# Optimization experiments

Hardware: AMD Instinct MI355X
Metric: run time of the kernel (lower is better)

Reference implementation:

```python
import jax, jax.numpy as jnp
import numpy as np

NUM_EXPERTS = 32
HIDDEN = 2048
INTER = 768
TOP_K = 4
B, S = 2, 512


def setup_inputs() -> dict:
    key = jax.random.key(0)
    k1, k2, k3, k4, k5 = jax.random.split(key, 5)
    hidden_states = jax.random.normal(k1, (B, S, HIDDEN), dtype=jnp.float32)
    routing_weights = jax.random.uniform(k2, (B, S, NUM_EXPERTS), dtype=jnp.float32)
    gate_up_proj = jax.random.normal(k3, (NUM_EXPERTS, HIDDEN, 2 * INTER), dtype=jnp.float32) * 0.02
    down_proj = jax.random.normal(k4, (NUM_EXPERTS, INTER, HIDDEN), dtype=jnp.float32) * 0.02
    router_indices = jax.random.randint(k5, (B, S, TOP_K), 0, NUM_EXPERTS, dtype=jnp.int64)
    return {
        "hidden_states": hidden_states,
        "routing_weights": routing_weights,
        "gate_up_proj": gate_up_proj,
        "down_proj": down_proj,
        "router_indices": router_indices,
    }


def reference(hidden_states, routing_weights, gate_up_proj, down_proj, router_indices):
    b, s, h = hidden_states.shape
    e = gate_up_proj.shape[0]
    x = hidden_states.reshape(-1, h)                       # [T, H]
    ri = router_indices.reshape(-1, router_indices.shape[-1])  # [T, K]
    rw = routing_weights.reshape(-1, e)                    # [T, E]
    # token-expert membership: expert applied once per token iff it appears in top-k
    member = (ri[:, :, None] == jnp.arange(e)[None, None, :]).any(axis=1)  # [T, E] bool
    combine_w = jnp.where(member, rw, 0.0)                 # [T, E]
    # dense grouped-GEMM reference: compute every expert for every token, mask-combine
    gate_up = jnp.einsum("th,ehg->teg", x, gate_up_proj)   # [T, E, 2I]
    gate, up = jnp.split(gate_up, 2, axis=-1)              # [T, E, I] each
    act = jax.nn.silu(gate) * up                           # SwiGLU
    act = act * combine_w[:, :, None]                      # fold combine weights pre-down-proj
    out = jnp.einsum("tei,eih->th", act, down_proj)        # [T, H]
    return out.reshape(b, s, h)
```

## Files before the change

### kernel.cpp

```cpp
#include <hip/hip_runtime.h>
#include <hip/hip_bf16.h>

#define NUM_EXPERTS 32
#define HIDDEN 2048
#define INTER 768
#define TOPK 4
#define T_TOKENS 1024
#define CAP 1024

#define MW 192
#define BK 64
#define LSTR 72

typedef __bf16 bf16x8 __attribute__((ext_vector_type(8)));
typedef float floatx4 __attribute__((ext_vector_type(4)));

__device__ __forceinline__ int swz(int row, int kq) {
    return row * LSTR + (((kq ^ (row >> 2)) & 7) << 3);
}

__global__ void route_kernel(const int* __restrict__ ri, int* __restrict__ counts,
                             int* __restrict__ tok_list) {
    int t = blockIdx.x * blockDim.x + threadIdx.x;
    if (t >= T_TOKENS) return;
    int idx[TOPK];
#pragma unroll
    for (int j = 0; j < TOPK; ++j) idx[j] = ri[t * TOPK + j];
#pragma unroll
    for (int j = 0; j < TOPK; ++j) {
        int e = idx[j];
        bool dup = false;
#pragma unroll
        for (int l = 0; l < TOPK; ++l)
            if (l < j && idx[l] == e) dup = true;
        if (!dup) {
            int s = atomicAdd(&counts[e], 1);
            tok_list[e * CAP + s] = t;
        }
    }
}

__global__ __launch_bounds__(256) void conv_kernel(const float* __restrict__ x,
                                                   __bf16* __restrict__ xb) {
    int i = (blockIdx.x * 256 + threadIdx.x) * 8;
    float4 f0 = *(const float4*)(x + i);
    float4 f1 = *(const float4*)(x + i + 4);
    bf16x8 p;
    p[0] = (__bf16)f0.x; p[1] = (__bf16)f0.y; p[2] = (__bf16)f0.z; p[3] = (__bf16)f0.w;
    p[4] = (__bf16)f1.x; p[5] = (__bf16)f1.y; p[6] = (__bf16)f1.z; p[7] = (__bf16)f1.w;
    *(bf16x8*)(xb + i) = p;
}

__global__ __launch_bounds__(256, 3) void gemm1_kernel(
    const __bf16* __restrict__ xb, const float* __restrict__ rw,
    const float* __restrict__ Wgu, const int* __restrict__ counts,
    const int* __restrict__ tok_list, __bf16* __restrict__ act) {
    const int e = blockIdx.y;
    const int n0 = blockIdx.x * 32;
    const int count = counts[e];
    const int tid = threadIdx.x;
    const int wave = tid >> 6;
    const int lane = tid & 63;
    const int fr = lane & 15;
    const int fq = lane >> 4;
    const int wr = wave >> 1;
    const int wc = wave & 1;

    __shared__ int s_off;
    __shared__ int s_tok[MW];
    __shared__ float s_w[MW];
    __shared__ __align__(16) __bf16 As[MW * LSTR];
    __shared__ __align__(16) __bf16 Bs[64 * LSTR];

    if (tid == 0) {
        int o = 0;
        for (int i = 0; i < e; ++i) o += counts[i];
        s_off = o;
    }

    const size_t wbase = (size_t)e * HIDDEN * (2 * INTER);

    const int brow = (tid & 31) * 2;
    const int kg = tid >> 5;
    const int bhalf = (brow >> 4) & 1;
    const int bcolm = n0 + ((brow >> 5) << 4) + (brow & 15) + (bhalf ? INTER : 0);
    const float* bCol = Wgu + wbase + (size_t)(kg * 8) * (2 * INTER) + bcolm;
    const int ar = tid >> 2;
    const int aq = tid & 3;

    for (int m0 = 0; m0 < count; m0 += MW) {
        __syncthreads();
        if (tid < MW) {
            int slot = m0 + tid;
            int t = (slot < count) ? tok_list[e * CAP + slot] : tok_list[e * CAP];
            s_tok[tid] = t;
            s_w[tid] = (slot < count) ? rw[t * NUM_EXPERTS + e] : 0.f;
        }
        __syncthreads();
        const int nt = min(3, (count - m0 + 63) >> 6);

        const __bf16* aRow[3];
#pragma unroll
        for (int mt = 0; mt < 3; ++mt)
            aRow[mt] = (mt < nt) ? (xb + (size_t)s_tok[mt * 64 + ar] * HIDDEN + aq * 16)
                                 : xb;

        bf16x8 qa[3][2];
        float2 qb[8];
        auto loadA = [&](int kb) {
#pragma unroll
            for (int mt = 0; mt < 3; ++mt)
                if (mt < nt) {
                    const bf16x8* s = (const bf16x8*)(aRow[mt] + kb);
                    qa[mt][0] = s[0];
                    qa[mt][1] = s[1];
                }
        };
        auto loadB = [&](int kb) {
#pragma unroll
            for (int r8 = 0; r8 < 8; ++r8)
                qb[r8] = *(const float2*)(bCol + (size_t)(kb + r8) * (2 * INTER));
        };
        auto writeA = [&]() {
#pragma unroll
            for (int mt = 0; mt < 3; ++mt)
                if (mt < nt) {
                    *(bf16x8*)&As[swz(mt * 64 + ar, 2 * aq)] = qa[mt][0];
                    *(bf16x8*)&As[swz(mt * 64 + ar, 2 * aq + 1)] = qa[mt][1];
                }
        };
        auto writeB = [&]() {
#pragma unroll
            for (int c = 0; c < 2; ++c) {
                bf16x8 p;
#pragma unroll
                for (int r8 = 0; r8 < 8; ++r8)
                    p[r8] = (__bf16)((const float*)&qb[r8])[c];
                *(bf16x8*)&Bs[swz(brow + c, kg)] = p;
            }
        };

        floatx4 acc[3][2][2];
#pragma unroll
        for (int mt = 0; mt < 3; ++mt)
#pragma unroll
            for (int ms = 0; ms < 2; ++ms)
#pragma unroll
                for (int nf = 0; nf < 2; ++nf)
                    acc[mt][ms][nf] = (floatx4){0.f, 0.f, 0.f, 0.f};

        loadA(0); loadB(0);
        writeA(); writeB();
        __syncthreads();

        for (int k0 = 0; k0 < HIDDEN; k0 += BK) {
            const bool hn = (k0 + BK < HIDDEN);
            if (hn) { loadA(k0 + BK); loadB(k0 + BK); }

#pragma unroll
            for (int ks = 0; ks < 2; ++ks) {
                bf16x8 bfr[2];
#pragma unroll
                for (int nf = 0; nf < 2; ++nf)
                    bfr[nf] = *(const bf16x8*)&Bs[swz(wc * 32 + nf * 16 + fr, ks * 4 + fq)];
#pragma unroll
                for (int mt = 0; mt < 3; ++mt)
                    if (mt < nt) {
                        bf16x8 af[2];
#pragma unroll
                        for (int ms = 0; ms < 2; ++ms)
                            af[ms] = *(const bf16x8*)&As[swz(mt * 64 + wr * 32 + ms * 16 + fr, ks * 4 + fq)];
#pragma unroll
                        for (int ms = 0; ms < 2; ++ms)
#pragma unroll
                            for (int nf = 0; nf < 2; ++nf)
                                acc[mt][ms][nf] = __builtin_amdgcn_mfma_f32_16x16x32_bf16(
                                    af[ms], bfr[nf], acc[mt][ms][nf], 0, 0, 0);
                    }
            }
            __syncthreads();
            if (hn) { writeA(); writeB(); }
            __syncthreads();
        }

        const int off = s_off;
#pragma unroll
        for (int mt = 0; mt < 3; ++mt)
            if (mt < nt) {
#pragma unroll
                for (int ms = 0; ms < 2; ++ms) {
                    int rb = mt * 64 + wr * 32 + ms * 16 + fq * 4;
#pragma unroll
                    for (int i = 0; i < 4; ++i) {
                        int slot = m0 + rb + i;
                        if (slot < count) {
                            float w = s_w[rb + i];
                            float gv = acc[mt][ms][0][i];
                            float uv = acc[mt][ms][1][i];
                            float a = gv / (1.f + __expf(-gv)) * uv * w;
                            act[(size_t)(off + slot) * INTER + n0 + wc * 16 + fr] = (__bf16)a;
                        }
                    }
                }
            }
    }
}

__global__ __launch_bounds__(256, 3) void gemm2_kernel(
    const __bf16* __restrict__ act, const float* __restrict__ Wd,
    const int* __restrict__ counts, const int* __restrict__ tok_list,
    float* __restrict__ out) {
    const int e = blockIdx.y;
    const int n0 = blockIdx.x * 64;
    const int count = counts[e];
    const int tid = threadIdx.x;
    const int wave = tid >> 6;
    const int lane = tid & 63;
    const int fr = lane & 15;
    const int fq = lane >> 4;
    const int wr = wave >> 1;
    const int wc = wave & 1;

    __shared__ int s_off;
    __shared__ int s_tok[MW];
    __shared__ __align__(16) __bf16 As[MW * LSTR];
    __shared__ __align__(16) __bf16 Bs[64 * LSTR];

    if (tid == 0) {
        int o = 0;
        for (int i = 0; i < e; ++i) o += counts[i];
        s_off = o;
    }

    const size_t wbase = (size_t)e * INTER * HIDDEN;
    const int brow = (tid & 31) * 2;
    const int kg = tid >> 5;
    const float* bCol = Wd + wbase + (size_t)(kg * 8) * HIDDEN + n0 + brow;
    const int ar = tid >> 2;
    const int aq = tid & 3;

    for (int m0 = 0; m0 < count; m0 += MW) {
        __syncthreads();
        if (tid < MW) {
            int slot = m0 + tid;
            s_tok[tid] = (slot < count) ? tok_list[e * CAP + slot] : 0;
        }
        __syncthreads();
        const int nt = min(3, (count - m0 + 63) >> 6);

        const __bf16* aRow[3];
#pragma unroll
        for (int mt = 0; mt < 3; ++mt)
            aRow[mt] = act + (size_t)(s_off + min(m0 + mt * 64 + ar, count - 1)) * INTER + aq * 16;

        bf16x8 qa[3][2];
        float2 qb[8];
        auto loadA = [&](int kb) {
#pragma unroll
            for (int mt = 0; mt < 3; ++mt)
                if (mt < nt) {
                    const bf16x8* s = (const bf16x8*)(aRow[mt] + kb);
                    qa[mt][0] = s[0];
                    qa[mt][1] = s[1];
                }
        };
        auto loadB = [&](int kb) {
#pragma unroll
            for (int r8 = 0; r8 < 8; ++r8)
                qb[r8] = *(const float2*)(bCol + (size_t)(kb + r8) * HIDDEN);
        };
        auto writeA = [&]() {
#pragma unroll
            for (int mt = 0; mt < 3; ++mt)
                if (mt < nt) {
                    *(bf16x8*)&As[swz(mt * 64 + ar, 2 * aq)] = qa[mt][0];
                    *(bf16x8*)&As[swz(mt * 64 + ar, 2 * aq + 1)] = qa[mt][1];
                }
        };
        auto writeB = [&]() {
#pragma unroll
            for (int c = 0; c < 2; ++c) {
                bf16x8 p;
#pragma unroll
                for (int r8 = 0; r8 < 8; ++r8)
                    p[r8] = (__bf16)((const float*)&qb[r8])[c];
                *(bf16x8*)&Bs[swz(brow + c, kg)] = p;
            }
        };

        floatx4 acc[3][2][2];
#pragma unroll
        for (int mt = 0; mt < 3; ++mt)
#pragma unroll
            for (int ms = 0; ms < 2; ++ms)
#pragma unroll
                for (int nf = 0; nf < 2; ++nf)
                    acc[mt][ms][nf] = (floatx4){0.f, 0.f, 0.f, 0.f};

        loadA(0); loadB(0);
        writeA(); writeB();
        __syncthreads();

        for (int k0 = 0; k0 < INTER; k0 += BK) {
            const bool hn = (k0 + BK < INTER);
            if (hn) { loadA(k0 + BK); loadB(k0 + BK); }

#pragma unroll
            for (int ks = 0; ks < 2; ++ks) {
                bf16x8 bfr[2];
#pragma unroll
                for (int nf = 0; nf < 2; ++nf)
                    bfr[nf] = *(const bf16x8*)&Bs[swz(wc * 32 + nf * 16 + fr, ks * 4 + fq)];
#pragma unroll
                for (int mt = 0; mt < 3; ++mt)
                    if (mt < nt) {
                        bf16x8 af[2];
#pragma unroll
                        for (int ms = 0; ms < 2; ++ms)
                            af[ms] = *(const bf16x8*)&As[swz(mt * 64 + wr * 32 + ms * 16 + fr, ks * 4 + fq)];
#pragma unroll
                        for (int ms = 0; ms < 2; ++ms)
#pragma unroll
                            for (int nf = 0; nf < 2; ++nf)
                                acc[mt][ms][nf] = __builtin_amdgcn_mfma_f32_16x16x32_bf16(
                                    af[ms], bfr[nf], acc[mt][ms][nf], 0, 0, 0);
                    }
            }
            __syncthreads();
            if (hn) { writeA(); writeB(); }
            __syncthreads();
        }

#pragma unroll
        for (int mt = 0; mt < 3; ++mt)
            if (mt < nt) {
#pragma unroll
                for (int ms = 0; ms < 2; ++ms) {
                    int rb = mt * 64 + wr * 32 + ms * 16 + fq * 4;
#pragma unroll
                    for (int i = 0; i < 4; ++i) {
                        int slot = m0 + rb + i;
                        if (slot < count) {
                            int t = s_tok[rb + i];
#pragma unroll
                            for (int nf = 0; nf < 2; ++nf)
                                atomicAdd(&out[(size_t)t * HIDDEN + n0 + wc * 32 + nf * 16 + fr],
                                          acc[mt][ms][nf][i]);
                        }
                    }
                }
            }
    }
}

extern "C" void kernel_launch(void* const* d_in, const int* in_sizes, int n_in,
                              void* d_out, int out_size, void* d_ws, size_t ws_size,
                              hipStream_t stream) {
    const float* x   = (const float*)d_in[0];
    const float* rw  = (const float*)d_in[1];
    const float* Wgu = (const float*)d_in[2];
    const float* Wd  = (const float*)d_in[3];
    const int*   ri  = (const int*)d_in[4];
    float* out = (float*)d_out;

    int* counts   = (int*)d_ws;
    int* tok_list = (int*)((char*)d_ws + 512);
    __bf16* act   = (__bf16*)((char*)d_ws + 512 + NUM_EXPERTS * CAP * 4);
    __bf16* xb    = (__bf16*)((char*)d_ws + 512 + NUM_EXPERTS * CAP * 4
                              + (size_t)NUM_EXPERTS * CAP * INTER * 2);

    hipMemsetAsync(d_ws, 0, 512, stream);
    hipMemsetAsync(d_out, 0, (size_t)T_TOKENS * HIDDEN * sizeof(float), stream);

    conv_kernel<<<dim3(T_TOKENS * HIDDEN / (256 * 8)), 256, 0, stream>>>(x, xb);
    route_kernel<<<dim3(T_TOKENS / 256), 256, 0, stream>>>(ri, counts, tok_list);
    gemm1_kernel<<<dim3(INTER / 32, NUM_EXPERTS), 256, 0, stream>>>(xb, rw, Wgu, counts, tok_list, act);
    gemm2_kernel<<<dim3(HIDDEN / 64, NUM_EXPERTS), 256, 0, stream>>>(act, Wd, counts, tok_list, out);
}
```

Before: 703.0 us.

## Replace atomic scatter-add in down-proj with partial buffer and per-token combine kernel

The down-projection kernel now writes per-slot results to a dense partial buffer instead of atomically adding into the output, and a new combine kernel gathers each token's up-to-four expert rows using an inverse map built during routing. The memsets are removed: counts are zeroed inside the conversion kernel, and the output no longer needs clearing because combine writes every element. The LDS swizzle is also changed to XOR with the low row bits. This trades float atomics and two memset launches for an extra kernel launch and a round trip of about 16 MB through the partial buffer.

```diff
diff --git a/kernel.cpp b/kernel.cpp
--- a/kernel.cpp
+++ b/kernel.cpp
@@ -16,32 +16,13 @@
 typedef float floatx4 __attribute__((ext_vector_type(4)));
 
 __device__ __forceinline__ int swz(int row, int kq) {
-    return row * LSTR + (((kq ^ (row >> 2)) & 7) << 3);
-}
-
-__global__ void route_kernel(const int* __restrict__ ri, int* __restrict__ counts,
-                             int* __restrict__ tok_list) {
-    int t = blockIdx.x * blockDim.x + threadIdx.x;
-    if (t >= T_TOKENS) return;
-    int idx[TOPK];
-#pragma unroll
-    for (int j = 0; j < TOPK; ++j) idx[j] = ri[t * TOPK + j];
-#pragma unroll
-    for (int j = 0; j < TOPK; ++j) {
-        int e = idx[j];
-        bool dup = false;
-#pragma unroll
-        for (int l = 0; l < TOPK; ++l)
-            if (l < j && idx[l] == e) dup = true;
-        if (!dup) {
-            int s = atomicAdd(&counts[e], 1);
-            tok_list[e * CAP + s] = t;
-        }
-    }
+    return row * LSTR + (((kq ^ (row & 7)) & 7) << 3);
 }
 
 __global__ __launch_bounds__(256) void conv_kernel(const float* __restrict__ x,
-                                                   __bf16* __restrict__ xb) {
+                                                   __bf16* __restrict__ xb,
+                                                   int* __restrict__ counts) {
+    if (blockIdx.x == 0 && threadIdx.x < NUM_EXPERTS) counts[threadIdx.x] = 0;
     int i = (blockIdx.x * 256 + threadIdx.x) * 8;
     float4 f0 = *(const float4*)(x + i);
     float4 f1 = *(const float4*)(x + i + 4);
@@ -49,6 +30,30 @@
     p[0] = (__bf16)f0.x; p[1] = (__bf16)f0.y; p[2] = (__bf16)f0.z; p[3] = (__bf16)f0.w;
     p[4] = (__bf16)f1.x; p[5] = (__bf16)f1.y; p[6] = (__bf16)f1.z; p[7] = (__bf16)f1.w;
     *(bf16x8*)(xb + i) = p;
+}
+
+__global__ void route_kernel(const int* __restrict__ ri, int* __restrict__ counts,
+                             int* __restrict__ tok_list, int* __restrict__ inv) {
+    int t = blockIdx.x * blockDim.x + threadIdx.x;
+    if (t >= T_TOKENS) return;
+    int idx[TOPK];
+#pragma unroll
+    for (int j = 0; j < TOPK; ++j) idx[j] = ri[t * TOPK + j];
+#pragma unroll
+    for (int j = 0; j < TOPK; ++j) {
+        int e = idx[j];
+        bool dup = false;
+#pragma unroll
+        for (int l = 0; l < TOPK; ++l)
+            if (l < j && idx[l] == e) dup = true;
+        if (!dup) {
+            int s = atomicAdd(&counts[e], 1);
+            tok_list[e * CAP + s] = t;
+            inv[t * TOPK + j] = (e << 16) | s;
+        } else {
+            inv[t * TOPK + j] = -1;
+        }
+    }
 }
 
 __global__ __launch_bounds__(256, 3) void gemm1_kernel(
@@ -209,7 +214,7 @@
 __global__ __launch_bounds__(256, 3) void gemm2_kernel(
     const __bf16* __restrict__ act, const float* __restrict__ Wd,
     const int* __restrict__ counts, const int* __restrict__ tok_list,
-    float* __restrict__ out) {
+    float* __restrict__ partial) {
     const int e = blockIdx.y;
     const int n0 = blockIdx.x * 64;
     const int count = counts[e];
@@ -222,7 +227,6 @@
     const int wc = wave & 1;
 
     __shared__ int s_off;
-    __shared__ int s_tok[MW];
     __shared__ __align__(16) __bf16 As[MW * LSTR];
     __shared__ __align__(16) __bf16 Bs[64 * LSTR];
 
@@ -231,6 +235,8 @@
         for (int i = 0; i < e; ++i) o += counts[i];
         s_off = o;
     }
+    __syncthreads();
+    const int off = s_off;
 
     const size_t wbase = (size_t)e * INTER * HIDDEN;
     const int brow = (tid & 31) * 2;
@@ -241,17 +247,12 @@
 
     for (int m0 = 0; m0 < count; m0 += MW) {
         __syncthreads();
-        if (tid < MW) {
-            int slot = m0 + tid;
-            s_tok[tid] = (slot < count) ? tok_list[e * CAP + slot] : 0;
-        }
-        __syncthreads();
         const int nt = min(3, (count - m0 + 63) >> 6);
 
         const __bf16* aRow[3];
 #pragma unroll
         for (int mt = 0; mt < 3; ++mt)
-            aRow[mt] = act + (size_t)(s_off + min(m0 + mt * 64 + ar, count - 1)) * INTER + aq * 16;
+            aRow[mt] = act + (size_t)(off + min(m0 + mt * 64 + ar, count - 1)) * INTER + aq * 16;
 
         bf16x8 qa[3][2];
         float2 qb[8];
@@ -341,16 +342,46 @@
                     for (int i = 0; i < 4; ++i) {
                         int slot = m0 + rb + i;
                         if (slot < count) {
-                            int t = s_tok[rb + i];
 #pragma unroll
                             for (int nf = 0; nf < 2; ++nf)
-                                atomicAdd(&out[(size_t)t * HIDDEN + n0 + wc * 32 + nf * 16 + fr],
-                                          acc[mt][ms][nf][i]);
+                                partial[(size_t)(off + slot) * HIDDEN + n0 + wc * 32 + nf * 16 + fr] =
+                                    acc[mt][ms][nf][i];
                         }
                     }
                 }
             }
     }
+}
+
+__global__ __launch_bounds__(256) void combine_kernel(
+    const float* __restrict__ partial, const int* __restrict__ counts,
+    const int* __restrict__ inv, float* __restrict__ out) {
+    const int t = blockIdx.x;
+    __shared__ int s_off[NUM_EXPERTS];
+    __shared__ int s_inv[TOPK];
+    if (threadIdx.x == 0) {
+        int o = 0;
+        for (int i = 0; i < NUM_EXPERTS; ++i) { s_off[i] = o; o += counts[i]; }
+    }
+    if (threadIdx.x < TOPK) s_inv[threadIdx.x] = inv[t * TOPK + threadIdx.x];
+    __syncthreads();
+    const int c0 = threadIdx.x * 8;
+    float4 a0 = {0.f, 0.f, 0.f, 0.f}, a1 = {0.f, 0.f, 0.f, 0.f};
+#pragma unroll
+    for (int j = 0; j < TOPK; ++j) {
+        int v = s_inv[j];
+        if (v >= 0) {
+            int e = v >> 16, s = v & 0xFFFF;
+            const float* p = partial + (size_t)(s_off[e] + s) * HIDDEN + c0;
+            float4 b0 = ((const float4*)p)[0];
+            float4 b1 = ((const float4*)p)[1];
+            a0.x += b0.x; a0.y += b0.y; a0.z += b0.z; a0.w += b0.w;
+            a1.x += b1.x; a1.y += b1.y; a1.z += b1.z; a1.w += b1.w;
+        }
+    }
+    float* o = out + (size_t)t * HIDDEN + c0;
+    ((float4*)o)[0] = a0;
+    ((float4*)o)[1] = a1;
 }
 
 extern "C" void kernel_launch(void* const* d_in, const int* in_sizes, int n_in,
@@ -363,17 +394,17 @@
     const int*   ri  = (const int*)d_in[4];
     float* out = (float*)d_out;
 
-    int* counts   = (int*)d_ws;
-    int* tok_list = (int*)((char*)d_ws + 512);
-    __bf16* act   = (__bf16*)((char*)d_ws + 512 + NUM_EXPERTS * CAP * 4);
-    __bf16* xb    = (__bf16*)((char*)d_ws + 512 + NUM_EXPERTS * CAP * 4
-                              + (size_t)NUM_EXPERTS * CAP * INTER * 2);
-
-    hipMemsetAsync(d_ws, 0, 512, stream);
-    hipMemsetAsync(d_out, 0, (size_t)T_TOKENS * HIDDEN * sizeof(float), stream);
-
-    conv_kernel<<<dim3(T_TOKENS * HIDDEN / (256 * 8)), 256, 0, stream>>>(x, xb);
-    route_kernel<<<dim3(T_TOKENS / 256), 256, 0, stream>>>(ri, counts, tok_list);
+    char* ws = (char*)d_ws;
+    int* counts    = (int*)ws;
+    int* tok_list  = (int*)(ws + 512);
+    __bf16* act    = (__bf16*)(ws + 512 + NUM_EXPERTS * CAP * 4);
+    __bf16* xb     = (__bf16*)((char*)act + (size_t)NUM_EXPERTS * CAP * INTER * 2);
+    int* inv       = (int*)((char*)xb + (size_t)T_TOKENS * HIDDEN * 2);
+    float* partial = (float*)((char*)inv + (size_t)T_TOKENS * TOPK * 4);
+
+    conv_kernel<<<dim3(T_TOKENS * HIDDEN / (256 * 8)), 256, 0, stream>>>(x, xb, counts);
+    route_kernel<<<dim3(T_TOKENS / 256), 256, 0, stream>>>(ri, counts, tok_list, inv);
     gemm1_kernel<<<dim3(INTER / 32, NUM_EXPERTS), 256, 0, stream>>>(xb, rw, Wgu, counts, tok_list, act);
-    gemm2_kernel<<<dim3(HIDDEN / 64, NUM_EXPERTS), 256, 0, stream>>>(act, Wd, counts, tok_list, out);
-}
+    gemm2_kernel<<<dim3(HIDDEN / 64, NUM_EXPERTS), 256, 0, stream>>>(act, Wd, counts, tok_list, partial);
+    combine_kernel<<<dim3(T_TOKENS), 256, 0, stream>>>(partial, counts, inv, out);
+}
```

After: 698.8 us. Within noise of the previous version (-0.6%).
